# Optimization experiments

Hardware: AMD Instinct MI355X
Metric: run time of the kernel (lower is better)

Reference implementation:

```python
import jax, jax.numpy as jnp
import numpy as np

DIM = 64
N_NODES = 20000
N_EDGES = 60000
N_TORS = 1024
ACT = 6


def setup_inputs() -> dict:
    key = jax.random.key(0)
    ks = iter(jax.random.split(key, 40))
    def rn(*s):
        return jax.random.normal(next(ks), s, dtype=jnp.float32) * 0.05
    d = DIM
    inp = {}
    inp["x"] = jax.random.normal(next(ks), (N_NODES, 3), dtype=jnp.float32)
    inp["edge_attr"] = jax.random.uniform(next(ks), (N_EDGES, 7), dtype=jnp.float32)
    inp["W0"] = rn(d, 3); inp["b0"] = rn(d)
    inp["We1"] = rn(128, 7); inp["be1"] = rn(128)
    inp["We2"] = rn(d * d, 128); inp["be2"] = rn(d * d)
    inp["root"] = rn(d, d); inp["conv_b"] = rn(d)
    inp["gru_wih"] = rn(3 * d, d); inp["gru_whh"] = rn(3 * d, d)
    inp["gru_bih"] = rn(3 * d); inp["gru_bhh"] = rn(3 * d)
    inp["s2s_wi"] = rn(4 * d, 2 * d); inp["s2s_wh"] = rn(4 * d, d)
    inp["s2s_bi"] = rn(4 * d); inp["s2s_bh"] = rn(4 * d)
    inp["mem_wi"] = rn(24 * d, 6 * d); inp["mem_wh"] = rn(24 * d, 6 * d)
    inp["mem_bi"] = rn(24 * d); inp["mem_bh"] = rn(24 * d)
    inp["W1"] = rn(2 * d, 6 * d); inp["b1"] = rn(2 * d)
    inp["W2"] = rn(ACT, 2 * d); inp["b2"] = rn(ACT)
    inp["edge_index"] = jax.random.randint(next(ks), (2, N_EDGES), 0, N_NODES)
    inp["nonring"] = jax.random.randint(next(ks), (N_TORS, 4), 0, N_NODES)
    return inp


def reference(x, edge_attr, W0, b0, We1, be1, We2, be2, root, conv_b,
              gru_wih, gru_whh, gru_bih, gru_bhh,
              s2s_wi, s2s_wh, s2s_bi, s2s_bh,
              mem_wi, mem_wh, mem_bi, mem_bh,
              W1, b1, W2, b2, edge_index, nonring):
    d = DIM
    n = x.shape[0]
    src, dst = edge_index[0], edge_index[1]
    # lin0 + relu
    out = jax.nn.relu(x @ W0.T + b0)                       # [N, d]
    h = out                                                # GRU hidden
    # per-edge dim x dim weights from the edge MLP (edge_attr is loop-invariant)
    We = jax.nn.relu(edge_attr @ We1.T + be1) @ We2.T + be2
    We = We.reshape(-1, d, d)                              # [E, d, d]
    deg = jnp.zeros((n,), jnp.float32).at[dst].add(1.0)
    inv_deg = 1.0 / jnp.maximum(deg, 1.0)
    for _ in range(6):
        # NNConv: gather -> per-edge matmul -> scatter-mean, plus root transform
        msg = jnp.einsum('ed,edf->ef', out[src], We)       # [E, d]
        agg = jnp.zeros((n, d), msg.dtype).at[dst].add(msg) * inv_deg[:, None]
        m = jax.nn.relu(agg + out @ root + conv_b)
        # GRU cell (torch gate order r, z, n)
        gx = m @ gru_wih.T + gru_bih
        gh = h @ gru_whh.T + gru_bhh
        r = jax.nn.sigmoid(gx[:, :d] + gh[:, :d])
        z = jax.nn.sigmoid(gx[:, d:2 * d] + gh[:, d:2 * d])
        nn_ = jnp.tanh(gx[:, 2 * d:] + r * gh[:, 2 * d:])
        h = (1.0 - z) * nn_ + z * h
        out = h
    # Set2Set pooling, single graph (data.batch is all zeros)
    q_star = jnp.zeros((1, 2 * d), out.dtype)
    hs = jnp.zeros((1, d), out.dtype)
    cs = jnp.zeros((1, d), out.dtype)
    for _ in range(6):
        g = q_star @ s2s_wi.T + s2s_bi + hs @ s2s_wh.T + s2s_bh
        i = jax.nn.sigmoid(g[:, :d])
        f = jax.nn.sigmoid(g[:, d:2 * d])
        gg = jnp.tanh(g[:, 2 * d:3 * d])
        o = jax.nn.sigmoid(g[:, 3 * d:])
        cs = f * cs + i * gg
        hs = o * jnp.tanh(cs)
        q = hs                                             # [1, d]
        e = out @ q[0]                                     # [N]
        a = jax.nn.softmax(e)
        rvec = (a[:, None] * out).sum(0, keepdims=True)    # [1, d]
        q_star = jnp.concatenate([q, rvec], axis=1)
    pool = q_star                                          # [1, 2d]
    # faithful quirky index/view/permute + repeat_interleave concat
    t = nonring.shape[0]
    sel = out[nonring.reshape(-1)]                         # [4T, d]
    sel = sel.reshape(4 * d, t).T                          # [T, 4d]
    rep = jnp.repeat(pool.reshape(-1), t).reshape(t, 2 * d)
    z_in = jnp.concatenate([sel, rep], axis=1)             # [T, 6d]
    # memory LSTM, seq_len = 1, zero initial state (states not passed in orig)
    D6 = 6 * d
    g = z_in @ mem_wi.T + mem_bi + mem_bh                  # h0 = 0 so Wh term vanishes
    i = jax.nn.sigmoid(g[:, :D6])
    f = jax.nn.sigmoid(g[:, D6:2 * D6])
    gg = jnp.tanh(g[:, 2 * D6:3 * D6])
    o = jax.nn.sigmoid(g[:, 3 * D6:])
    cm = i * gg
    hm = o * jnp.tanh(cm)                                  # [T, 6d]
    y = jax.nn.relu(hm @ W1.T + b1) @ W2.T + b2            # [T, ACT]
    return y[None]                                         # [1, T, ACT]
```

## Files before the change

### kernel.cpp

```cpp
#include <hip/hip_runtime.h>
#include <hip/hip_bf16.h>

#define NN 20000
#define NE 60000
#define NT 1024

typedef unsigned short ushortT;
typedef __attribute__((ext_vector_type(8))) short bf16x8;
typedef __attribute__((ext_vector_type(8))) unsigned short u16x8;
typedef __attribute__((ext_vector_type(4))) float f32x4;

__device__ __forceinline__ float sigm(float x){ return 1.0f/(1.0f+expf(-x)); }
__device__ __forceinline__ float bfu2f(ushortT u){ return __uint_as_float(((unsigned)u)<<16); }
__device__ __forceinline__ ushortT f2bfu(float f){
  __hip_bfloat16 b = __float2bfloat16(f);
  return *reinterpret_cast<ushortT*>(&b);
}

__global__ void k_lin0(const float* __restrict__ x, const float* __restrict__ W0,
                       const float* __restrict__ b0, float* __restrict__ out,
                       float* __restrict__ h, ushortT* __restrict__ outbf,
                       ushortT* __restrict__ hbf){
  int idx = blockIdx.x*256 + threadIdx.x;
  int n = idx >> 6, j = idx & 63;
  float a = b0[j] + x[n*3+0]*W0[j*3+0] + x[n*3+1]*W0[j*3+1] + x[n*3+2]*W0[j*3+2];
  a = fmaxf(a, 0.0f);
  out[idx] = a; h[idx] = a;
  ushortT u = f2bfu(a);
  outbf[idx] = u; hbf[idx] = u;
}

__global__ void k_deg(const int* __restrict__ dst, float* __restrict__ deg){
  int e = blockIdx.x*256 + threadIdx.x;
  if (e < NE) atomicAdd(&deg[dst[e]], 1.0f);
}

__global__ void k_edgemlp(const float* __restrict__ ea, const float* __restrict__ We1,
                          const float* __restrict__ be1, ushortT* __restrict__ Rbf){
  int idx = blockIdx.x*256 + threadIdx.x;
  int e = idx >> 7, k = idx & 127;
  float a = be1[k];
  #pragma unroll
  for (int j = 0; j < 7; ++j) a += ea[e*7+j]*We1[k*7+j];
  Rbf[idx] = f2bfu(fmaxf(a, 0.0f));
}

#define PREP_T ((4096*128) + (1536*384) + (128*384) + (192*64) + (192*64) + (64*64))
__global__ void k_prep(const float* __restrict__ We2, const float* __restrict__ memwi,
                       const float* __restrict__ W1, const float* __restrict__ gwih,
                       const float* __restrict__ gwhh, const float* __restrict__ root,
                       ushortT* __restrict__ We2bf, ushortT* __restrict__ wmem,
                       ushortT* __restrict__ w1bf, ushortT* __restrict__ gwihbf,
                       ushortT* __restrict__ gwhhbf, ushortT* __restrict__ rootTbf){
  int idx = blockIdx.x*256 + threadIdx.x;
  if (idx < 4096*128){ We2bf[idx] = f2bfu(We2[idx]); return; }
  idx -= 4096*128;
  if (idx < 1536*384){ wmem[idx] = f2bfu(memwi[idx]); return; }
  idx -= 1536*384;
  if (idx < 128*384){ w1bf[idx] = f2bfu(W1[idx]); return; }
  idx -= 128*384;
  if (idx < 192*64){ gwihbf[idx] = f2bfu(gwih[idx]); return; }
  idx -= 192*64;
  if (idx < 192*64){ gwhhbf[idx] = f2bfu(gwhh[idx]); return; }
  idx -= 192*64;
  if (idx < 64*64){ int d = idx >> 6, j = idx & 63; rootTbf[j*64 + d] = f2bfu(root[idx]); }
}

#define EB 256
__global__ __launch_bounds__(256, 2) void k_fmsg(
    const ushortT* __restrict__ Rbf, const ushortT* __restrict__ We2bf,
    const float* __restrict__ be2, const ushortT* __restrict__ outbf,
    const int* __restrict__ src, const int* __restrict__ dst,
    float* __restrict__ agg)
{
  __shared__ ushortT o_sT[64][264];
  __shared__ ushortT bufB[4][4096];
  __shared__ float   be2q[64][32];
  __shared__ int     dst_s[EB];

  int tid = threadIdx.x;
  int e0 = blockIdx.x * EB;
  int fh = blockIdx.y;
  int w = tid >> 6, lane = tid & 63;
  int l15 = lane & 15, g = lane >> 4;

  auto stage = [&](int d, int b){
    #pragma unroll
    for (int i = 0; i < 2; ++i){
      int s = (w*2 + i)*64 + lane;
      int row = s >> 4, kslot = s & 15;
      const ushortT* gp = We2bf + (size_t)((d<<6) + (fh<<5) + row)*128 + ((kslot ^ (row & 7))<<3);
      __builtin_amdgcn_global_load_lds(
          (const __attribute__((address_space(1))) void*)gp,
          (__attribute__((address_space(3))) void*)&bufB[b][(size_t)s*8], 16, 0, 0);
    }
  };
  stage(0, 0); stage(1, 1); stage(2, 2);

  {
    int ge = e0 + tid;
    int sn = src[ge];
    dst_s[tid] = (ge < NE) ? dst[ge] : -1;
    const ushortT* op = outbf + (size_t)sn*64;
    #pragma unroll
    for (int i = 0; i < 8; ++i){
      u16x8 v = *reinterpret_cast<const u16x8*>(op + i*8);
      #pragma unroll
      for (int j = 0; j < 8; ++j) o_sT[i*8+j][tid] = v[j];
    }
  }
  #pragma unroll
  for (int i = 0; i < 8; ++i){
    int idx = tid*8 + i;
    int dd = idx >> 5, cc = idx & 31;
    be2q[dd][cc] = be2[(dd<<6) + (fh<<5) + cc];
  }

  bf16x8 af[4][4];
  #pragma unroll
  for (int t = 0; t < 4; ++t){
    #pragma unroll
    for (int ks = 0; ks < 4; ++ks){
      int ge = e0 + w*64 + t*16 + l15;
      bf16x8 z = {0,0,0,0,0,0,0,0};
      af[t][ks] = (ge < NE) ? *reinterpret_cast<const bf16x8*>(Rbf + (size_t)ge*128 + ks*32 + g*8) : z;
    }
  }

  f32x4 msg[4][2];
  #pragma unroll
  for (int t = 0; t < 4; ++t){
    #pragma unroll
    for (int q = 0; q < 2; ++q){ msg[t][q][0]=0.f; msg[t][q][1]=0.f; msg[t][q][2]=0.f; msg[t][q][3]=0.f; }
  }
  __syncthreads();

  auto compute = [&](int d, int b){
    bf16x8 bf0[4], bf1[4];
    #pragma unroll
    for (int ks = 0; ks < 4; ++ks){
      bf0[ks] = *reinterpret_cast<const bf16x8*>(&bufB[b][ (l15)*128    + ((((ks<<2)+g) ^ (l15&7))<<3) ]);
      bf1[ks] = *reinterpret_cast<const bf16x8*>(&bufB[b][ (16+l15)*128 + ((((ks<<2)+g) ^ (l15&7))<<3) ]);
    }
    f32x4 ac[4][2];
    #pragma unroll
    for (int t = 0; t < 4; ++t){
      #pragma unroll
      for (int q = 0; q < 2; ++q){ ac[t][q][0]=0.f; ac[t][q][1]=0.f; ac[t][q][2]=0.f; ac[t][q][3]=0.f; }
    }
    __builtin_amdgcn_s_setprio(1);
    #pragma unroll
    for (int ks = 0; ks < 4; ++ks){
      #pragma unroll
      for (int t = 0; t < 4; ++t){
        ac[t][0] = __builtin_amdgcn_mfma_f32_16x16x32_bf16(af[t][ks], bf0[ks], ac[t][0], 0, 0, 0);
        ac[t][1] = __builtin_amdgcn_mfma_f32_16x16x32_bf16(af[t][ks], bf1[ks], ac[t][1], 0, 0, 0);
      }
    }
    __builtin_amdgcn_s_setprio(0);
    float be2v0 = be2q[d][l15];
    float be2v1 = be2q[d][16 + l15];
    #pragma unroll
    for (int t = 0; t < 4; ++t){
      ushort4 ou = *reinterpret_cast<const ushort4*>(&o_sT[d][w*64 + t*16 + g*4]);
      float o0 = bfu2f(ou.x), o1 = bfu2f(ou.y), o2 = bfu2f(ou.z), o3 = bfu2f(ou.w);
      msg[t][0][0] += o0*(ac[t][0][0] + be2v0);
      msg[t][0][1] += o1*(ac[t][0][1] + be2v0);
      msg[t][0][2] += o2*(ac[t][0][2] + be2v0);
      msg[t][0][3] += o3*(ac[t][0][3] + be2v0);
      msg[t][1][0] += o0*(ac[t][1][0] + be2v1);
      msg[t][1][1] += o1*(ac[t][1][1] + be2v1);
      msg[t][1][2] += o2*(ac[t][1][2] + be2v1);
      msg[t][1][3] += o3*(ac[t][1][3] + be2v1);
    }
  };

  for (int d = 0; d < 61; ++d){
    asm volatile("s_waitcnt vmcnt(4)" ::: "memory");
    __builtin_amdgcn_sched_barrier(0);
    __builtin_amdgcn_s_barrier();
    __builtin_amdgcn_sched_barrier(0);
    stage(d + 3, (d + 3) & 3);
    compute(d, d & 3);
  }
  asm volatile("s_waitcnt vmcnt(4)" ::: "memory");
  __builtin_amdgcn_sched_barrier(0);
  __builtin_amdgcn_s_barrier();
  __builtin_amdgcn_sched_barrier(0);
  compute(61, 61 & 3);
  asm volatile("s_waitcnt vmcnt(2)" ::: "memory");
  __builtin_amdgcn_sched_barrier(0);
  __builtin_amdgcn_s_barrier();
  __builtin_amdgcn_sched_barrier(0);
  compute(62, 62 & 3);
  asm volatile("s_waitcnt vmcnt(0)" ::: "memory");
  __builtin_amdgcn_sched_barrier(0);
  __builtin_amdgcn_s_barrier();
  __builtin_amdgcn_sched_barrier(0);
  compute(63, 63 & 3);

  #pragma unroll
  for (int t = 0; t < 4; ++t){
    #pragma unroll
    for (int r = 0; r < 4; ++r){
      int el = w*64 + t*16 + g*4 + r;
      int tn = dst_s[el];
      if (tn >= 0){
        atomicAdd(&agg[(size_t)tn*64 + (fh<<5) + l15],      msg[t][0][r]);
        atomicAdd(&agg[(size_t)tn*64 + (fh<<5) + 16 + l15], msg[t][1][r]);
      }
    }
  }
}

__global__ __launch_bounds__(256) void k_gru2(
    const float* __restrict__ agg_in, const float* __restrict__ deg,
    const ushortT* __restrict__ rootT, const float* __restrict__ conv_b,
    const ushortT* __restrict__ wih, const ushortT* __restrict__ whh,
    const float* __restrict__ bih, const float* __restrict__ bhh,
    float* __restrict__ out, float* __restrict__ h,
    ushortT* __restrict__ outbf, ushortT* __restrict__ hbf)
{
  __shared__ ushortT mbf[32*64];
  float* agg = const_cast<float*>(agg_in);
  int tid = threadIdx.x;
  int w = tid >> 6, lane = tid & 63;
  int l15 = lane & 15, g = lane >> 4;
  int n0 = blockIdx.x * 32;
  int j = w*16 + l15;

  f32x4 acc1[2];
  #pragma unroll
  for (int rt = 0; rt < 2; ++rt){ acc1[rt][0]=0.f; acc1[rt][1]=0.f; acc1[rt][2]=0.f; acc1[rt][3]=0.f; }
  bf16x8 ah[2][2];
  #pragma unroll
  for (int ks = 0; ks < 2; ++ks){
    bf16x8 b = *reinterpret_cast<const bf16x8*>(rootT + (size_t)j*64 + g*8 + ks*32);
    #pragma unroll
    for (int rt = 0; rt < 2; ++rt){
      bf16x8 a = *reinterpret_cast<const bf16x8*>(outbf + (size_t)(n0 + rt*16 + l15)*64 + g*8 + ks*32);
      acc1[rt] = __builtin_amdgcn_mfma_f32_16x16x32_bf16(a, b, acc1[rt], 0, 0, 0);
      ah[rt][ks] = *reinterpret_cast<const bf16x8*>(hbf + (size_t)(n0 + rt*16 + l15)*64 + g*8 + ks*32);
    }
  }
  {
    float cb = conv_b[j];
    #pragma unroll
    for (int rt = 0; rt < 2; ++rt){
      #pragma unroll
      for (int r = 0; r < 4; ++r){
        int row = rt*16 + g*4 + r;
        int node = n0 + row;
        float inv = 1.0f/fmaxf(deg[node], 1.0f);
        float mval = fmaxf(acc1[rt][r] + agg[(size_t)node*64 + j]*inv + cb, 0.0f);
        agg[(size_t)node*64 + j] = 0.0f;
        int gran = (j >> 3) ^ (row & 7);
        mbf[row*64 + (gran<<3) + (j & 7)] = f2bfu(mval);
      }
    }
  }
  __syncthreads();

  f32x4 gx[3][2], gh[3][2];
  #pragma unroll
  for (int ci = 0; ci < 3; ++ci){
    #pragma unroll
    for (int rt = 0; rt < 2; ++rt){
      gx[ci][rt][0]=0.f; gx[ci][rt][1]=0.f; gx[ci][rt][2]=0.f; gx[ci][rt][3]=0.f;
      gh[ci][rt][0]=0.f; gh[ci][rt][1]=0.f; gh[ci][rt][2]=0.f; gh[ci][rt][3]=0.f;
    }
  }
  #pragma unroll
  for (int ks = 0; ks < 2; ++ks){
    bf16x8 am[2];
    #pragma unroll
    for (int rt = 0; rt < 2; ++rt){
      int arow = rt*16 + l15;
      int agran = (g + ks*4) ^ (l15 & 7);
      am[rt] = *reinterpret_cast<const bf16x8*>(&mbf[arow*64 + (agran<<3)]);
    }
    #pragma unroll
    for (int ci = 0; ci < 3; ++ci){
      int c = (w + ci*4)*16 + l15;
      bf16x8 bx = *reinterpret_cast<const bf16x8*>(wih + (size_t)c*64 + g*8 + ks*32);
      bf16x8 bh = *reinterpret_cast<const bf16x8*>(whh + (size_t)c*64 + g*8 + ks*32);
      #pragma unroll
      for (int rt = 0; rt < 2; ++rt){
        gx[ci][rt] = __builtin_amdgcn_mfma_f32_16x16x32_bf16(am[rt], bx, gx[ci][rt], 0, 0, 0);
        gh[ci][rt] = __builtin_amdgcn_mfma_f32_16x16x32_bf16(ah[rt][ks], bh, gh[ci][rt], 0, 0, 0);
      }
    }
  }
  float bxr = bih[j], bxz = bih[64+j], bxn = bih[128+j];
  float bhr = bhh[j], bhz = bhh[64+j], bhn = bhh[128+j];
  #pragma unroll
  for (int rt = 0; rt < 2; ++rt){
    #pragma unroll
    for (int r = 0; r < 4; ++r){
      int node = n0 + rt*16 + g*4 + r;
      float gxr = gx[0][rt][r] + bxr, gxz = gx[1][rt][r] + bxz, gxn = gx[2][rt][r] + bxn;
      float ghr = gh[0][rt][r] + bhr, ghz = gh[1][rt][r] + bhz, ghn = gh[2][rt][r] + bhn;
      float rr = sigm(gxr + ghr), zz = sigm(gxz + ghz);
      float nn_ = tanhf(gxn + rr*ghn);
      float hold = h[(size_t)node*64 + j];
      float hn = (1.0f - zz)*nn_ + zz*hold;
      h[(size_t)node*64 + j]   = hn;
      out[(size_t)node*64 + j] = hn;
      ushortT u = f2bfu(hn);
      outbf[(size_t)node*64 + j] = u;
      hbf[(size_t)node*64 + j]   = u;
    }
  }
}

__global__ void k_s2s2(const float* __restrict__ out, const float* __restrict__ wi,
                       const float* __restrict__ wh, const float* __restrict__ bi,
                       const float* __restrict__ bh, float* __restrict__ st, int it){
  const float* sr = st + it*256;
  float* sw = st + (it+1)*256;
  __shared__ float qs[128], hsl[64], gg[256];
  __shared__ float ob[128*65], wl[128], zred[128], part[256];
  int tid = threadIdx.x;
  int n0 = blockIdx.x * 128;

  if (tid < 64) qs[tid] = sr[tid];
  else if (tid < 128){
    float Z = sr[192];
    qs[tid] = (Z != 0.0f) ? sr[128 + (tid-64)]/Z : 0.0f;
  }
  __syncthreads();
  {
    float a = bi[tid] + bh[tid];
    #pragma unroll 8
    for (int k = 0; k < 128; ++k) a += qs[k]*wi[tid*128 + k];
    #pragma unroll 8
    for (int k = 0; k < 64;  ++k) a += sr[k]*wh[tid*64 + k];
    gg[tid] = a;
  }
  __syncthreads();
  if (tid < 64){
    float iv = sigm(gg[tid]), fv = sigm(gg[64+tid]);
    float gv = tanhf(gg[128+tid]), ov = sigm(gg[192+tid]);
    float c = fv*sr[64+tid] + iv*gv;
    float hnew = ov*tanhf(c);
    hsl[tid] = hnew;
    if (blockIdx.x == 0){ sw[64+tid] = c; sw[tid] = hnew; }
  }
  #pragma unroll
  for (int rr = 0; rr < 8; ++rr){
    int idx = rr*1024 + tid*4;
    int nl = idx >> 6, jj = idx & 63;
    float4 v = make_float4(0.f,0.f,0.f,0.f);
    if (n0 + nl < NN) v = *reinterpret_cast<const float4*>(&out[(size_t)(n0+nl)*64 + jj]);
    ob[nl*65 + jj + 0] = v.x; ob[nl*65 + jj + 1] = v.y;
    ob[nl*65 + jj + 2] = v.z; ob[nl*65 + jj + 3] = v.w;
  }
  __syncthreads();
  if (tid < 128){
    float e = 0.f;
    #pragma unroll 8
    for (int jj = 0; jj < 64; ++jj) e += ob[tid*65 + jj]*hsl[jj];
    float wv = (n0 + tid < NN) ? expf(e) : 0.f;
    wl[tid] = wv; zred[tid] = wv;
  }
  __syncthreads();
  if (tid < 64) zred[tid] += zred[tid + 64];
  __syncthreads();
  if (tid < 32) zred[tid] += zred[tid + 32];
  __syncthreads();
  if (tid < 16) zred[tid] += zred[tid + 16];
  __syncthreads();
  if (tid < 8) zred[tid] += zred[tid + 8];
  __syncthreads();
  if (tid == 0){
    float z = zred[0]+zred[1]+zred[2]+zred[3]+zred[4]+zred[5]+zred[6]+zred[7];
    atomicAdd(&sw[192], z);
  }
  {
    int gq = tid >> 6, d = tid & 63;
    float acc = 0.f;
    #pragma unroll 8
    for (int i = 0; i < 32; ++i){
      int nl = gq*32 + i;
      acc += wl[nl]*ob[nl*65 + d];
    }
    part[tid] = acc;
  }
  __syncthreads();
  if (tid < 64)
    atomicAdd(&sw[128 + tid], part[tid] + part[64+tid] + part[128+tid] + part[192+tid]);
}

__global__ void k_z(const float* __restrict__ out, const float* __restrict__ st,
                    const int* __restrict__ nonring, ushortT* __restrict__ zbf){
  const float* s6 = st + 6*256;
  int idx = blockIdx.x*256 + threadIdx.x;
  int t = idx / 384, c = idx % 384;
  float v;
  if (c < 256){
    int a = c*16 + (t >> 6);
    int node = nonring[a];
    v = out[(size_t)node*64 + (t & 63)];
  } else {
    int pi = t >> 3;
    v = (pi < 64) ? s6[pi] : s6[128 + (pi - 64)] / s6[192];
  }
  zbf[idx] = f2bfu(v);
}

__global__ __launch_bounds__(256) void k_mem2(
    const ushortT* __restrict__ zbf, const ushortT* __restrict__ wmem,
    const float* __restrict__ membi, const float* __restrict__ membh,
    ushortT* __restrict__ hmbf){
  int tid = threadIdx.x;
  int w = tid >> 6, lane = tid & 63;
  int l15 = lane & 15, g = lane >> 4;
  int m0 = blockIdx.x * 32;
  int jw = blockIdx.y * 64 + w * 16;

  f32x4 ai[2], ag[2], ao[2];
  #pragma unroll
  for (int m = 0; m < 2; ++m){
    #pragma unroll
    for (int r = 0; r < 4; ++r){ ai[m][r]=0.f; ag[m][r]=0.f; ao[m][r]=0.f; }
  }
  const ushortT* a0p = zbf + (size_t)(m0 + l15)*384 + g*8;
  const ushortT* a1p = zbf + (size_t)(m0 + 16 + l15)*384 + g*8;
  const ushortT* bip = wmem + (size_t)(jw + l15)*384 + g*8;
  const ushortT* bgp = wmem + (size_t)(768 + jw + l15)*384 + g*8;
  const ushortT* bop = wmem + (size_t)(1152 + jw + l15)*384 + g*8;
  #pragma unroll
  for (int ks = 0; ks < 12; ++ks){
    bf16x8 a0 = *reinterpret_cast<const bf16x8*>(a0p + ks*32);
    bf16x8 a1 = *reinterpret_cast<const bf16x8*>(a1p + ks*32);
    bf16x8 bi = *reinterpret_cast<const bf16x8*>(bip + ks*32);
    bf16x8 bg = *reinterpret_cast<const bf16x8*>(bgp + ks*32);
    bf16x8 bo = *reinterpret_cast<const bf16x8*>(bop + ks*32);
    ai[0] = __builtin_amdgcn_mfma_f32_16x16x32_bf16(a0, bi, ai[0], 0, 0, 0);
    ai[1] = __builtin_amdgcn_mfma_f32_16x16x32_bf16(a1, bi, ai[1], 0, 0, 0);
    ag[0] = __builtin_amdgcn_mfma_f32_16x16x32_bf16(a0, bg, ag[0], 0, 0, 0);
    ag[1] = __builtin_amdgcn_mfma_f32_16x16x32_bf16(a1, bg, ag[1], 0, 0, 0);
    ao[0] = __builtin_amdgcn_mfma_f32_16x16x32_bf16(a0, bo, ao[0], 0, 0, 0);
    ao[1] = __builtin_amdgcn_mfma_f32_16x16x32_bf16(a1, bo, ao[1], 0, 0, 0);
  }
  int j = jw + l15;
  float bI = membi[j]        + membh[j];
  float bG = membi[768 + j]  + membh[768 + j];
  float bO = membi[1152 + j] + membh[1152 + j];
  #pragma unroll
  for (int m = 0; m < 2; ++m){
    #pragma unroll
    for (int r = 0; r < 4; ++r){
      int t = m0 + m*16 + g*4 + r;
      float gi = ai[m][r] + bI;
      float gG = ag[m][r] + bG;
      float go = ao[m][r] + bO;
      float cm = sigm(gi)*tanhf(gG);
      hmbf[(size_t)t*384 + j] = f2bfu(sigm(go)*tanhf(cm));
    }
  }
}

__global__ __launch_bounds__(256) void k_fin1(
    const ushortT* __restrict__ hmbf, const ushortT* __restrict__ w1bf,
    const float* __restrict__ b1, float* __restrict__ hid){
  int tid = threadIdx.x;
  int w = tid >> 6, lane = tid & 63;
  int l15 = lane & 15, g = lane >> 4;
  int m0 = blockIdx.x * 32;
  int cw = blockIdx.y * 64 + w * 16;

  f32x4 acc[2];
  #pragma unroll
  for (int m = 0; m < 2; ++m){
    #pragma unroll
    for (int r = 0; r < 4; ++r) acc[m][r] = 0.f;
  }
  const ushortT* a0p = hmbf + (size_t)(m0 + l15)*384 + g*8;
  const ushortT* a1p = hmbf + (size_t)(m0 + 16 + l15)*384 + g*8;
  const ushortT* bp  = w1bf + (size_t)(cw + l15)*384 + g*8;
  #pragma unroll
  for (int ks = 0; ks < 12; ++ks){
    bf16x8 a0 = *reinterpret_cast<const bf16x8*>(a0p + ks*32);
    bf16x8 a1 = *reinterpret_cast<const bf16x8*>(a1p + ks*32);
    bf16x8 b  = *reinterpret_cast<const bf16x8*>(bp + ks*32);
    acc[0] = __builtin_amdgcn_mfma_f32_16x16x32_bf16(a0, b, acc[0], 0, 0, 0);
    acc[1] = __builtin_amdgcn_mfma_f32_16x16x32_bf16(a1, b, acc[1], 0, 0, 0);
  }
  int c = cw + l15;
  float bv = b1[c];
  #pragma unroll
  for (int m = 0; m < 2; ++m){
    #pragma unroll
    for (int r = 0; r < 4; ++r){
      int t = m0 + m*16 + g*4 + r;
      hid[(size_t)t*128 + c] = fmaxf(acc[m][r] + bv, 0.0f);
    }
  }
}

__global__ void k_fin2(const float* __restrict__ hid, const float* __restrict__ W2,
                       const float* __restrict__ b2, float* __restrict__ y){
  int tid = threadIdx.x;
  int t = blockIdx.x*32 + (tid >> 3);
  int j = tid & 7;
  if (j >= 6) return;
  float a = b2[j];
  const float* hp = hid + (size_t)t*128;
  const float* wp = W2 + j*128;
  #pragma unroll 8
  for (int k = 0; k < 128; ++k) a += hp[k]*wp[k];
  y[t*6 + j] = a;
}

extern "C" void kernel_launch(void* const* d_in, const int* in_sizes, int n_in,
                              void* d_out, int out_size, void* d_ws, size_t ws_size,
                              hipStream_t stream){
  const float* x      = (const float*)d_in[0];
  const float* ea     = (const float*)d_in[1];
  const float* W0     = (const float*)d_in[2];
  const float* b0     = (const float*)d_in[3];
  const float* We1    = (const float*)d_in[4];
  const float* be1    = (const float*)d_in[5];
  const float* We2    = (const float*)d_in[6];
  const float* be2    = (const float*)d_in[7];
  const float* root   = (const float*)d_in[8];
  const float* conv_b = (const float*)d_in[9];
  const float* gwih   = (const float*)d_in[10];
  const float* gwhh   = (const float*)d_in[11];
  const float* gbih   = (const float*)d_in[12];
  const float* gbhh   = (const float*)d_in[13];
  const float* s2swi  = (const float*)d_in[14];
  const float* s2swh  = (const float*)d_in[15];
  const float* s2sbi  = (const float*)d_in[16];
  const float* s2sbh  = (const float*)d_in[17];
  const float* memwi  = (const float*)d_in[18];
  const float* membi  = (const float*)d_in[20];
  const float* membh  = (const float*)d_in[21];
  const float* W1     = (const float*)d_in[22];
  const float* b1     = (const float*)d_in[23];
  const float* W2     = (const float*)d_in[24];
  const float* b2     = (const float*)d_in[25];
  const int*   eidx   = (const int*)d_in[26];
  const int*   nonr   = (const int*)d_in[27];
  const int* src = eidx, *dst = eidx + NE;
  float* y = (float*)d_out;

  char* wsb = (char*)d_ws;
  size_t off = 0;
  auto alloc = [&](size_t bytes){ size_t o = off; off += (bytes + 255) & ~(size_t)255; return o; };
  float* out    = (float*)(wsb + alloc((size_t)NN*64*4));
  float* h      = (float*)(wsb + alloc((size_t)NN*64*4));
  float* agg    = (float*)(wsb + alloc((size_t)NN*64*4));
  float* deg    = (float*)(wsb + alloc((size_t)NN*4));
  float* st     = (float*)(wsb + alloc(7*256*4));
  float* hid    = (float*)(wsb + alloc((size_t)NT*128*4));
  ushortT* Rbf  = (ushortT*)(wsb + alloc((size_t)NE*128*2));
  ushortT* We2bf= (ushortT*)(wsb + alloc((size_t)4096*128*2));
  ushortT* wmem = (ushortT*)(wsb + alloc((size_t)1536*384*2));
  ushortT* w1bf = (ushortT*)(wsb + alloc((size_t)128*384*2));
  ushortT* zbf  = (ushortT*)(wsb + alloc((size_t)NT*384*2));
  ushortT* hmbf = (ushortT*)(wsb + alloc((size_t)NT*384*2));
  ushortT* outbf= (ushortT*)(wsb + alloc((size_t)NN*64*2));
  ushortT* hbf  = (ushortT*)(wsb + alloc((size_t)NN*64*2));
  ushortT* gwihbf = (ushortT*)(wsb + alloc((size_t)192*64*2));
  ushortT* gwhhbf = (ushortT*)(wsb + alloc((size_t)192*64*2));
  ushortT* rootTbf= (ushortT*)(wsb + alloc((size_t)64*64*2));
  (void)ws_size; (void)n_in; (void)in_sizes; (void)out_size;

  hipMemsetAsync(deg, 0, (size_t)NN*4, stream);
  hipMemsetAsync(st, 0, 7*256*4, stream);
  hipMemsetAsync(agg, 0, (size_t)NN*64*4, stream);
  k_lin0<<<NN*64/256, 256, 0, stream>>>(x, W0, b0, out, h, outbf, hbf);
  k_deg<<<(NE+255)/256, 256, 0, stream>>>(dst, deg);
  k_edgemlp<<<NE*128/256, 256, 0, stream>>>(ea, We1, be1, Rbf);
  k_prep<<<(PREP_T+255)/256, 256, 0, stream>>>(We2, memwi, W1, gwih, gwhh, root,
                                               We2bf, wmem, w1bf, gwihbf, gwhhbf, rootTbf);

  for (int it = 0; it < 6; ++it){
    k_fmsg<<<dim3((NE + EB - 1)/EB, 2), 256, 0, stream>>>(Rbf, We2bf, be2, outbf, src, dst, agg);
    k_gru2<<<NN/32, 256, 0, stream>>>(agg, deg, rootTbf, conv_b, gwihbf, gwhhbf,
                                      gbih, gbhh, out, h, outbf, hbf);
  }

  for (int it = 0; it < 6; ++it){
    k_s2s2<<<(NN + 127)/128, 256, 0, stream>>>(out, s2swi, s2swh, s2sbi, s2sbh, st, it);
  }

  k_z<<<NT*384/256, 256, 0, stream>>>(out, st, nonr, zbf);
  k_mem2<<<dim3(32, 6), 256, 0, stream>>>(zbf, wmem, membi, membh, hmbf);
  k_fin1<<<dim3(32, 2), 256, 0, stream>>>(hmbf, w1bf, b1, hid);
  k_fin2<<<32, 256, 0, stream>>>(hid, W2, b2, y);
}
```

Baseline: 680.1 us.

## Load We2 B-fragments directly into registers instead of LDS staging

Replaces the four-deep LDS ring buffer of We2 tiles, filled with global_load_lds and synchronized by per-iteration barriers, with direct global loads of B fragments into registers, double-buffered across d iterations. This removes the per-step workgroup barriers and the LDS traffic and frees 32KB of shared memory, which may allow higher occupancy. The trade-off is that each wave now loads the same We2 data redundantly from global/L2 instead of sharing it through LDS, and register pressure rises from holding two buffers of B fragments.

```diff
diff --git a/kernel.cpp b/kernel.cpp
--- a/kernel.cpp
+++ b/kernel.cpp
@@ -74,7 +74,6 @@
     float* __restrict__ agg)
 {
   __shared__ ushortT o_sT[64][264];
-  __shared__ ushortT bufB[4][4096];
   __shared__ float   be2q[64][32];
   __shared__ int     dst_s[EB];
 
@@ -84,19 +83,6 @@
   int w = tid >> 6, lane = tid & 63;
   int l15 = lane & 15, g = lane >> 4;
 
-  auto stage = [&](int d, int b){
-    #pragma unroll
-    for (int i = 0; i < 2; ++i){
-      int s = (w*2 + i)*64 + lane;
-      int row = s >> 4, kslot = s & 15;
-      const ushortT* gp = We2bf + (size_t)((d<<6) + (fh<<5) + row)*128 + ((kslot ^ (row & 7))<<3);
-      __builtin_amdgcn_global_load_lds(
-          (const __attribute__((address_space(1))) void*)gp,
-          (__attribute__((address_space(3))) void*)&bufB[b][(size_t)s*8], 16, 0, 0);
-    }
-  };
-  stage(0, 0); stage(1, 1); stage(2, 2);
-
   {
     int ge = e0 + tid;
     int sn = src[ge];
@@ -135,13 +121,20 @@
   }
   __syncthreads();
 
-  auto compute = [&](int d, int b){
-    bf16x8 bf0[4], bf1[4];
+  const ushortT* bp0 = We2bf + (size_t)((fh<<5) + l15)*128 + g*8;
+  const ushortT* bp1 = We2bf + (size_t)((fh<<5) + 16 + l15)*128 + g*8;
+  const int DSTRIDE = 64*128;
+
+  bf16x8 bA[8], bB[8];
+  auto loadB = [&](const ushortT* p0, const ushortT* p1, bf16x8* bb){
     #pragma unroll
     for (int ks = 0; ks < 4; ++ks){
-      bf0[ks] = *reinterpret_cast<const bf16x8*>(&bufB[b][ (l15)*128    + ((((ks<<2)+g) ^ (l15&7))<<3) ]);
-      bf1[ks] = *reinterpret_cast<const bf16x8*>(&bufB[b][ (16+l15)*128 + ((((ks<<2)+g) ^ (l15&7))<<3) ]);
-    }
+      bb[ks]     = *reinterpret_cast<const bf16x8*>(p0 + ks*32);
+      bb[4 + ks] = *reinterpret_cast<const bf16x8*>(p1 + ks*32);
+    }
+  };
+
+  auto domfma = [&](int d, const bf16x8* bb){
     f32x4 ac[4][2];
     #pragma unroll
     for (int t = 0; t < 4; ++t){
@@ -153,8 +146,8 @@
     for (int ks = 0; ks < 4; ++ks){
       #pragma unroll
       for (int t = 0; t < 4; ++t){
-        ac[t][0] = __builtin_amdgcn_mfma_f32_16x16x32_bf16(af[t][ks], bf0[ks], ac[t][0], 0, 0, 0);
-        ac[t][1] = __builtin_amdgcn_mfma_f32_16x16x32_bf16(af[t][ks], bf1[ks], ac[t][1], 0, 0, 0);
+        ac[t][0] = __builtin_amdgcn_mfma_f32_16x16x32_bf16(af[t][ks], bb[ks],     ac[t][0], 0, 0, 0);
+        ac[t][1] = __builtin_amdgcn_mfma_f32_16x16x32_bf16(af[t][ks], bb[4 + ks], ac[t][1], 0, 0, 0);
       }
     }
     __builtin_amdgcn_s_setprio(0);
@@ -175,29 +168,16 @@
     }
   };
 
-  for (int d = 0; d < 61; ++d){
-    asm volatile("s_waitcnt vmcnt(4)" ::: "memory");
-    __builtin_amdgcn_sched_barrier(0);
-    __builtin_amdgcn_s_barrier();
-    __builtin_amdgcn_sched_barrier(0);
-    stage(d + 3, (d + 3) & 3);
-    compute(d, d & 3);
-  }
-  asm volatile("s_waitcnt vmcnt(4)" ::: "memory");
-  __builtin_amdgcn_sched_barrier(0);
-  __builtin_amdgcn_s_barrier();
-  __builtin_amdgcn_sched_barrier(0);
-  compute(61, 61 & 3);
-  asm volatile("s_waitcnt vmcnt(2)" ::: "memory");
-  __builtin_amdgcn_sched_barrier(0);
-  __builtin_amdgcn_s_barrier();
-  __builtin_amdgcn_sched_barrier(0);
-  compute(62, 62 & 3);
-  asm volatile("s_waitcnt vmcnt(0)" ::: "memory");
-  __builtin_amdgcn_sched_barrier(0);
-  __builtin_amdgcn_s_barrier();
-  __builtin_amdgcn_sched_barrier(0);
-  compute(63, 63 & 3);
+  loadB(bp0, bp1, bA); bp0 += DSTRIDE; bp1 += DSTRIDE;
+  for (int d = 0; d < 62; d += 2){
+    loadB(bp0, bp1, bB); bp0 += DSTRIDE; bp1 += DSTRIDE;
+    domfma(d, bA);
+    loadB(bp0, bp1, bA); bp0 += DSTRIDE; bp1 += DSTRIDE;
+    domfma(d + 1, bB);
+  }
+  loadB(bp0, bp1, bB);
+  domfma(62, bA);
+  domfma(63, bB);
 
   #pragma unroll
   for (int t = 0; t < 4; ++t){
```

Measured after the change: 1.080 ms. 58.9% more time.
